# Kernel optimization log

Measured on AMD Instinct MI355X. Metric: run time of the kernel, lower is better.

## Reference

```python
import jax, jax.numpy as jnp
import numpy as np

OFFSET = 1  # self.offset

def setup_inputs() -> dict:
    key = jax.random.key(0)
    k1, k2, k3, k4, k5 = jax.random.split(key, 5)
    B, D, T, S, N = 16, 512, 1024, 12, 10
    x = jax.random.normal(k1, (B, D, T), dtype=jnp.float32)
    y = jax.random.normal(k2, (B, D, T), dtype=jnp.float32)
    W = jax.random.normal(k3, (D, D, S), dtype=jnp.float32) * 0.05  # ConvTranspose2d weight [in, out, 1, steps] squeezed
    b = jax.random.normal(k4, (D,), dtype=jnp.float32) * 0.05
    neg_idxs = jax.random.randint(k5, (B, N * T), 0, T)
    return {"x": x, "y": y, "W": W, "b": b, "neg_idxs": neg_idxs}


def reference(x, y, W, b, neg_idxs):
    B, F, T = y.shape
    N = neg_idxs.shape[1] // T
    # --- sample_negatives: gather by computed index over flattened y ---
    y_flat = jnp.transpose(y, (1, 0, 2)).reshape(F, B * T)          # [F, B*T]
    idx = (neg_idxs + jnp.arange(B, dtype=neg_idxs.dtype)[:, None] * T).reshape(-1)
    negs = y_flat[:, idx].reshape(F, B, N, T).transpose(2, 1, 0, 3)  # [N, B, F, T]
    targets = jnp.concatenate([y[None], negs], axis=0)               # [C=N+1, B, F, T]
    # --- project_to_steps: ConvTranspose2d with kernel (1, steps) == per-step linear ---
    xp = jnp.einsum('bit,ios->bots', x, W) + b[None, :, None, None]  # [B, F, T, S]
    C = N + 1
    S = xp.shape[-1]
    steps = min(S, T - OFFSET)
    preds, labels = [], []
    for i in range(steps):  # small fixed loop over prediction steps
        off = i + OFFSET
        # [C, B, T-off]: dot over feature dim, copies broadcast over x
        p = jnp.einsum('bft,cbft->cbt', xp[:, :, :T - off, i], targets[:, :, :, off:])
        preds.append(p.reshape(-1))
        lab = jnp.zeros((C, B * (T - off)), dtype=xp.dtype).at[0].set(1.0)
        labels.append(lab.reshape(-1))
    predictions = jnp.concatenate(preds)
    labels_out = jnp.concatenate(labels)
    return predictions, labels_out
```

## Files before the change

### kernel.cpp

```cpp
#include <hip/hip_runtime.h>

typedef __bf16 bf16x8 __attribute__((ext_vector_type(8)));
typedef float f32x4 __attribute__((ext_vector_type(4)));

#define B_ 16
#define T_ 1024
#define D_ 512
#define S_ 12
#define C_ 11
static constexpr int P_TOTAL = 2148960;

__device__ __host__ inline constexpr int pred_base(int i) {
  return C_ * B_ * (T_ * i - (i * (i + 1)) / 2);
}

__device__ inline unsigned short f2bf(float f) {
  unsigned int u = __float_as_uint(f);
  u += 0x7FFF + ((u >> 16) & 1);
  return (unsigned short)(u >> 16);
}

__device__ inline void gld16(const void* g, void* l) {
  __builtin_amdgcn_global_load_lds(
      (const __attribute__((address_space(1))) void*)g,
      (__attribute__((address_space(3))) void*)l, 16, 0, 0);
}

__global__ __launch_bounds__(256) void prep_w(const float* __restrict__ W,
                                              unsigned short* __restrict__ wt) {
  __shared__ unsigned short tile[32][33][12];
  const int i0 = blockIdx.x * 32, o0 = blockIdx.y * 32;
#pragma unroll
  for (int q = 0; q < 48; ++q) {
    int idx = threadIdx.x + q * 256;
    int ii = idx / 384, rem = idx % 384;
    tile[ii][rem / 12][rem % 12] =
        f2bf(W[(size_t)(i0 + ii) * 6144 + (size_t)o0 * 12 + rem]);
  }
  __syncthreads();
#pragma unroll
  for (int q = 0; q < 48; ++q) {
    int idx = threadIdx.x + q * 256;
    int ss = idx / 1024, rem = idx % 1024;
    int oo = rem / 32, ii = rem % 32;
    wt[(size_t)ss * (D_ * D_) + (size_t)(o0 + oo) * D_ + (i0 + ii)] = tile[ii][oo][ss];
  }
}

__global__ __launch_bounds__(256) void prep_t2(const float* __restrict__ xin,
                                               const float* __restrict__ yin,
                                               unsigned short* __restrict__ xo,
                                               unsigned short* __restrict__ yo) {
  __shared__ float tile[32][33];
  const int t0 = blockIdx.x * 32;
  const int d0 = blockIdx.y * 32;
  const int b = blockIdx.z & 15;
  const float* in = (blockIdx.z < 16) ? xin : yin;
  unsigned short* ob = (blockIdx.z < 16) ? xo : yo;
  const float* ib = in + (size_t)b * D_ * T_;
  const int r = threadIdx.x / 32, c = threadIdx.x % 32;
#pragma unroll
  for (int p = 0; p < 4; ++p) {
    int rr = r + p * 8;
    tile[rr][c] = ib[(size_t)(d0 + rr) * T_ + t0 + c];
  }
  __syncthreads();
  unsigned short* op = ob + (size_t)b * T_ * D_;
#pragma unroll
  for (int p = 0; p < 4; ++p) {
    int rr = r + p * 8;
    op[(size_t)(t0 + rr) * D_ + d0 + c] = f2bf(tile[c][rr]);
  }
}

__global__ void labels_k(float* __restrict__ lab) {
  int k = blockIdx.x * 256 + threadIdx.x;
  if (k >= P_TOTAL) return;
  int i = 0;
#pragma unroll
  for (int q = 1; q < 12; ++q)
    if (k >= pred_base(q)) i = q;
  int rel = k - pred_base(i);
  int len = T_ - 1 - i;
  lab[k] = (rel < B_ * len) ? 1.0f : 0.0f;
}

__global__ __launch_bounds__(512, 2) void gemm_xp(
    const unsigned short* __restrict__ xb,
    const unsigned short* __restrict__ wt,
    const float* __restrict__ bias,
    unsigned short* __restrict__ xp,
    int tiles, int mtiles) {
  __shared__ unsigned short lds[65536];
  const int tid = threadIdx.x;
  const int w = tid >> 6, l = tid & 63;
  const int gm = w >> 2, gn = w & 3;
  const int fr = l & 15, sgrp = l >> 4;

  const int so0 = tid * 16;
  const int row0 = so0 >> 6, sc0 = (so0 >> 4) & 3;
  const int go0 = row0 * 1024 + ((sc0 ^ ((row0 >> 1) & 3)) << 4);
  const int so1 = so0 + 8192;
  const int row1 = so1 >> 6, sc1 = (so1 >> 4) & 3;
  const int go1 = row1 * 1024 + ((sc1 ^ ((row1 >> 1) & 3)) << 4);

  auto stage = [&](const unsigned short* srcKt, int slotShorts) {
    gld16((const char*)srcKt + go0, (char*)&lds[slotShorts] + so0);
    gld16((const char*)srcKt + go1, (char*)&lds[slotShorts] + so1);
  };

  int aOff[2][4], bOff[4];
#pragma unroll
  for (int ms = 0; ms < 2; ++ms)
#pragma unroll
    for (int fm = 0; fm < 4; ++fm) {
      int row = gm * 128 + ms * 64 + fm * 16 + fr;
      aOff[ms][fm] = row * 32 + ((sgrp ^ ((row >> 1) & 3)) << 3);
    }
#pragma unroll
  for (int fn = 0; fn < 4; ++fn) {
    int row = gn * 64 + fn * 16 + fr;
    bOff[fn] = row * 32 + ((sgrp ^ ((row >> 1) & 3)) << 3);
  }

  auto decode = [&](int t, const unsigned short*& Ag, const unsigned short*& Bg,
                    int& n0v, int& miv, int& siv) {
    miv = t % mtiles;
    int rest = t / mtiles;
    int ni = rest & 1;
    siv = rest >> 1;
    Ag = xb + (size_t)(miv * 256) * D_;
    Bg = wt + ((size_t)siv * D_ + ni * 256) * D_;
    n0v = ni * 256;
  };

  int ti = blockIdx.x;
  if (ti >= tiles) return;
  const unsigned short *Ag, *Bg, *Agn = nullptr, *Bgn = nullptr;
  int n0, mi, si, n0n, min_, sin_;
  decode(ti, Ag, Bg, n0, mi, si);
  int tin = ti + gridDim.x;
  bool hasNext = tin < tiles;
  if (hasNext) decode(tin, Agn, Bgn, n0n, min_, sin_);

  stage(Ag, 0);
  stage(Bg, 8192);
  stage(Ag + 32, 16384);
  stage(Bg + 32, 16384 + 8192);
  asm volatile("s_waitcnt vmcnt(4)" ::: "memory");
  __builtin_amdgcn_s_barrier();

  bf16x8 afA[4], bfrA[4];
#pragma unroll
  for (int fn = 0; fn < 4; ++fn)
    bfrA[fn] = *(const bf16x8*)&lds[8192 + bOff[fn]];
#pragma unroll
  for (int fm = 0; fm < 4; ++fm)
    afA[fm] = *(const bf16x8*)&lds[aOff[0][fm]];

  while (true) {
    f32x4 acc[2][4][4];
#pragma unroll
    for (int ms = 0; ms < 2; ++ms)
#pragma unroll
      for (int fm = 0; fm < 4; ++fm)
#pragma unroll
        for (int fn = 0; fn < 4; ++fn)
#pragma unroll
          for (int e = 0; e < 4; ++e) acc[ms][fm][fn][e] = 0.f;

    float bv[4];
#pragma unroll
    for (int fn = 0; fn < 4; ++fn) bv[fn] = bias[n0 + gn * 64 + fn * 16 + fr];

#pragma unroll
    for (int kt = 0; kt < 16; ++kt) {
      const int sl = (kt & 3) * 16384;
      bf16x8 afB[4];
#pragma unroll
      for (int fm = 0; fm < 4; ++fm)
        afB[fm] = *(const bf16x8*)&lds[sl + aOff[1][fm]];

      const int k2 = kt + 2;
      const int sl2 = (k2 & 3) * 16384;
      bool st = false;
      if (k2 < 16) {
        stage(Ag + k2 * 32, sl2);
        stage(Bg + k2 * 32, sl2 + 8192);
        st = true;
      } else if (hasNext) {
        stage(Agn + (k2 - 16) * 32, sl2);
        stage(Bgn + (k2 - 16) * 32, sl2 + 8192);
        st = true;
      }

      __builtin_amdgcn_s_setprio(1);
#pragma unroll
      for (int fm = 0; fm < 4; ++fm)
#pragma unroll
        for (int fn = 0; fn < 4; ++fn)
          acc[0][fm][fn] = __builtin_amdgcn_mfma_f32_16x16x32_bf16(
              afA[fm], bfrA[fn], acc[0][fm][fn], 0, 0, 0);
      __builtin_amdgcn_s_setprio(0);

      if (st) {
        asm volatile("s_waitcnt vmcnt(4)" ::: "memory");
      } else if (kt == 14) {
        asm volatile("s_waitcnt vmcnt(0)" ::: "memory");
      }
      __builtin_amdgcn_s_barrier();

      bf16x8 afN[4], bfN[4];
      const bool pre = (kt < 15) || hasNext;
      if (pre) {
        const int nsl = ((kt + 1) & 3) * 16384;
#pragma unroll
        for (int fn = 0; fn < 4; ++fn)
          bfN[fn] = *(const bf16x8*)&lds[nsl + 8192 + bOff[fn]];
#pragma unroll
        for (int fm = 0; fm < 4; ++fm)
          afN[fm] = *(const bf16x8*)&lds[nsl + aOff[0][fm]];
      }

      __builtin_amdgcn_s_setprio(1);
#pragma unroll
      for (int fm = 0; fm < 4; ++fm)
#pragma unroll
        for (int fn = 0; fn < 4; ++fn)
          acc[1][fm][fn] = __builtin_amdgcn_mfma_f32_16x16x32_bf16(
              afB[fm], bfrA[fn], acc[1][fm][fn], 0, 0, 0);
      __builtin_amdgcn_s_setprio(0);

      if (pre) {
#pragma unroll
        for (int fm = 0; fm < 4; ++fm) afA[fm] = afN[fm];
#pragma unroll
        for (int fn = 0; fn < 4; ++fn) bfrA[fn] = bfN[fn];
      }
    }

#pragma unroll
    for (int ms = 0; ms < 2; ++ms) {
#pragma unroll
      for (int fm = 0; fm < 4; ++fm) {
#pragma unroll
        for (int r = 0; r < 4; ++r) {
          int m = mi * 256 + gm * 128 + ms * 64 + fm * 16 + sgrp * 4 + r;
          int bl = m >> 10, t = m & 1023;
          size_t orow = (((size_t)bl * S_ + si) * T_ + t) * D_;
#pragma unroll
          for (int fn = 0; fn < 4; ++fn) {
            int o = n0 + gn * 64 + fn * 16 + fr;
            xp[orow + o] = f2bf(acc[ms][fm][fn][r] + bv[fn]);
          }
        }
      }
    }

    if (!hasNext) break;
    ti = tin;
    Ag = Agn; Bg = Bgn; n0 = n0n; mi = min_; si = sin_;
    tin = ti + gridDim.x;
    hasNext = tin < tiles;
    if (hasNext) decode(tin, Agn, Bgn, n0n, min_, sin_);
  }
}

__global__ __launch_bounds__(256) void pred_k(
    const unsigned short* __restrict__ xp,
    const unsigned short* __restrict__ yT,
    const int* __restrict__ negs,
    float* __restrict__ preds, int b0) {
  const int w = threadIdx.x >> 6, l = threadIdx.x & 63;
  const int bl = blockIdx.y;
  const int b = b0 + bl;
  const int fr = l & 15;
  const int koff = (l >> 4) * 8;

  const unsigned short* arow[4];
  const unsigned short* brow[4];
  int tts[4];
#pragma unroll
  for (int q = 0; q < 4; ++q) {
    int tt = blockIdx.x * 4 + w + q * 256;
    tts[q] = tt;
    int t = tt - 1 - fr;
    bool av = (fr < S_) && (t >= 0);
    arow[q] = xp + (((size_t)bl * S_ + (av ? fr : 0)) * T_ + (av ? t : 0)) * D_;
    int j = tt;
    if (fr >= 1 && fr <= 10) j = negs[b * (10 * T_) + (fr - 1) * T_ + tt];
    brow[q] = yT + ((size_t)b * T_ + j) * D_;
  }

  f32x4 acc[4];
#pragma unroll
  for (int q = 0; q < 4; ++q)
#pragma unroll
    for (int e = 0; e < 4; ++e) acc[q][e] = 0.f;

#pragma unroll
  for (int kk = 0; kk < 16; ++kk) {
#pragma unroll
    for (int q = 0; q < 4; ++q) {
      bf16x8 a = *(const bf16x8*)(arow[q] + kk * 32 + koff);
      bf16x8 bb = *(const bf16x8*)(brow[q] + kk * 32 + koff);
      acc[q] = __builtin_amdgcn_mfma_f32_16x16x32_bf16(a, bb, acc[q], 0, 0, 0);
    }
  }

#pragma unroll
  for (int q = 0; q < 4; ++q) {
#pragma unroll
    for (int r = 0; r < 4; ++r) {
      int ii = (l >> 4) * 4 + r;
      int to = tts[q] - 1 - ii;
      if (ii < S_ && fr < C_ && tts[q] >= 1 && to >= 0) {
        int len = T_ - 1 - ii;
        preds[pred_base(ii) + ((size_t)fr * B_ + b) * len + to] = acc[q][r];
      }
    }
  }
}

extern "C" void kernel_launch(void* const* d_in, const int* in_sizes, int n_in,
                              void* d_out, int out_size, void* d_ws, size_t ws_size,
                              hipStream_t stream) {
  (void)in_sizes; (void)n_in; (void)out_size;
  const float* x = (const float*)d_in[0];
  const float* y = (const float*)d_in[1];
  const float* W = (const float*)d_in[2];
  const float* bias = (const float*)d_in[3];
  const int* negs = (const int*)d_in[4];
  float* out = (float*)d_out;
  char* ws = (char*)d_ws;

  unsigned short* wt = (unsigned short*)ws;
  unsigned short* xb = (unsigned short*)(ws + 6291456);
  unsigned short* yT = (unsigned short*)(ws + 6291456 + 16777216);
  unsigned short* xp = (unsigned short*)(ws + 6291456 + 2 * 16777216);
  const size_t fixed = 6291456 + (size_t)2 * 16777216;
  const size_t xp_per_b = (size_t)S_ * T_ * D_ * 2;
  int nb = 1;
  if (ws_size > fixed) {
    size_t cap = (ws_size - fixed) / xp_per_b;
    nb = cap < 1 ? 1 : (cap > 16 ? 16 : (int)cap);
  }

  hipLaunchKernelGGL(prep_w, dim3(16, 16), dim3(256), 0, stream, W, wt);
  hipLaunchKernelGGL(prep_t2, dim3(32, 16, 32), dim3(256), 0, stream, x, y, xb, yT);
  hipLaunchKernelGGL(labels_k, dim3((P_TOTAL + 255) / 256), dim3(256), 0, stream,
                     out + P_TOTAL);

  for (int b0 = 0; b0 < B_; b0 += nb) {
    int bc = (B_ - b0) < nb ? (B_ - b0) : nb;
    int tiles = bc * 4 * 2 * 12;
    int grid = tiles < 256 ? tiles : 256;
    hipLaunchKernelGGL(gemm_xp, dim3(grid), dim3(512), 0, stream,
                       xb + (size_t)b0 * T_ * D_, wt, bias, xp,
                       tiles, bc * 4);
    hipLaunchKernelGGL(pred_k, dim3(64, bc), dim3(256), 0, stream,
                       xp, yT, negs, out, b0);
  }
}
```

Baseline: 220.6 us.

## Retile projection GEMM to 256x128 tiles with XCD-aware scheduling and triple buffering

Shrinks the gemm_xp block from 512 to 256 threads and the output tile from 256x256 to 256x128. The LDS ring goes from four 32-wide K stages to three 64-wide stages (72 KB), so two blocks can fit per CU. Tile indices are reordered so each XCD handles a contiguous chunk of M-major tiles, aiming for better L2 reuse of the weights and activations. The cost is more tiles, with A loaded twice as often per output column, and different register and LDS pressure.

Result: slower. 259.2 us (+17.5%).

```diff
diff --git a/kernel.cpp b/kernel.cpp
--- a/kernel.cpp
+++ b/kernel.cpp
@@ -85,78 +85,96 @@
   lab[k] = (rel < B_ * len) ? 1.0f : 0.0f;
 }
 
-__global__ __launch_bounds__(512, 2) void gemm_xp(
+__global__ __launch_bounds__(256, 2) void gemm_xp(
     const unsigned short* __restrict__ xb,
     const unsigned short* __restrict__ wt,
     const float* __restrict__ bias,
     unsigned short* __restrict__ xp,
-    int tiles, int mtiles) {
-  __shared__ unsigned short lds[65536];
+    int tiles, int chunk, int bpx) {
+  __shared__ unsigned short lds[36864];
   const int tid = threadIdx.x;
   const int w = tid >> 6, l = tid & 63;
-  const int gm = w >> 2, gn = w & 3;
+  const int gm = w >> 1, gn = w & 1;
   const int fr = l & 15, sgrp = l >> 4;
 
-  const int so0 = tid * 16;
-  const int row0 = so0 >> 6, sc0 = (so0 >> 4) & 3;
-  const int go0 = row0 * 1024 + ((sc0 ^ ((row0 >> 1) & 3)) << 4);
-  const int so1 = so0 + 8192;
-  const int row1 = so1 >> 6, sc1 = (so1 >> 4) & 3;
-  const int go1 = row1 * 1024 + ((sc1 ^ ((row1 >> 1) & 3)) << 4);
-
-  auto stage = [&](const unsigned short* srcKt, int slotShorts) {
-    gld16((const char*)srcKt + go0, (char*)&lds[slotShorts] + so0);
-    gld16((const char*)srcKt + go1, (char*)&lds[slotShorts] + so1);
+  int soA[4], goA[4], soB[2], goB[2];
+#pragma unroll
+  for (int seg = 0; seg < 4; ++seg) {
+    soA[seg] = tid * 16 + seg * 4096;
+    int row = soA[seg] >> 6, sc = (soA[seg] >> 4) & 3;
+    goA[seg] = row * 1024 + ((sc ^ ((row >> 1) & 3)) << 4);
+  }
+#pragma unroll
+  for (int seg = 0; seg < 2; ++seg) {
+    soB[seg] = tid * 16 + seg * 4096;
+    int row = soB[seg] >> 6, sc = (soB[seg] >> 4) & 3;
+    goB[seg] = row * 1024 + ((sc ^ ((row >> 1) & 3)) << 4);
+  }
+
+  auto stage = [&](const unsigned short* Akt, const unsigned short* Bkt, int slotB) {
+#pragma unroll
+    for (int seg = 0; seg < 4; ++seg)
+      gld16((const char*)Akt + goA[seg], (char*)lds + slotB + soA[seg]);
+#pragma unroll
+    for (int seg = 0; seg < 2; ++seg)
+      gld16((const char*)Bkt + goB[seg], (char*)lds + slotB + 16384 + soB[seg]);
   };
 
-  int aOff[2][4], bOff[4];
-#pragma unroll
-  for (int ms = 0; ms < 2; ++ms)
-#pragma unroll
-    for (int fm = 0; fm < 4; ++fm) {
-      int row = gm * 128 + ms * 64 + fm * 16 + fr;
-      aOff[ms][fm] = row * 32 + ((sgrp ^ ((row >> 1) & 3)) << 3);
-    }
+  int aOff[8], bOff[4];
+#pragma unroll
+  for (int fm = 0; fm < 8; ++fm) {
+    int row = gm * 128 + fm * 16 + fr;
+    aOff[fm] = row * 64 + ((sgrp ^ ((row >> 1) & 3)) << 4);
+  }
 #pragma unroll
   for (int fn = 0; fn < 4; ++fn) {
     int row = gn * 64 + fn * 16 + fr;
-    bOff[fn] = row * 32 + ((sgrp ^ ((row >> 1) & 3)) << 3);
-  }
+    bOff[fn] = 16384 + row * 64 + ((sgrp ^ ((row >> 1) & 3)) << 4);
+  }
+
+  auto rdf = [&](int slotB, int off) -> bf16x8 {
+    return *(const bf16x8*)((const char*)lds + slotB + off);
+  };
 
   auto decode = [&](int t, const unsigned short*& Ag, const unsigned short*& Bg,
                     int& n0v, int& miv, int& siv) {
-    miv = t % mtiles;
-    int rest = t / mtiles;
-    int ni = rest & 1;
-    siv = rest >> 1;
+    miv = t / 48;
+    int r = t % 48;
+    int ni = r & 3;
+    siv = r >> 2;
     Ag = xb + (size_t)(miv * 256) * D_;
-    Bg = wt + ((size_t)siv * D_ + ni * 256) * D_;
-    n0v = ni * 256;
+    Bg = wt + ((size_t)siv * D_ + ni * 128) * D_;
+    n0v = ni * 128;
   };
 
-  int ti = blockIdx.x;
-  if (ti >= tiles) return;
+  const int xcd = blockIdx.x & 7;
+  const int idx = blockIdx.x >> 3;
+  const int limit = (xcd + 1) * chunk;
+  int ti = xcd * chunk + idx;
+  if (ti >= limit || ti >= tiles) return;
+
   const unsigned short *Ag, *Bg, *Agn = nullptr, *Bgn = nullptr;
   int n0, mi, si, n0n, min_, sin_;
   decode(ti, Ag, Bg, n0, mi, si);
-  int tin = ti + gridDim.x;
-  bool hasNext = tin < tiles;
+  int tin = ti + bpx;
+  bool hasNext = tin < limit;
   if (hasNext) decode(tin, Agn, Bgn, n0n, min_, sin_);
 
-  stage(Ag, 0);
-  stage(Bg, 8192);
-  stage(Ag + 32, 16384);
-  stage(Bg + 32, 16384 + 8192);
-  asm volatile("s_waitcnt vmcnt(4)" ::: "memory");
+  int rdB = 0, stB = 2 * 24576;
+  auto adv = [](int s) { return s == 2 * 24576 ? 0 : s + 24576; };
+
+  stage(Ag, Bg, 0);
+  stage(Ag + 32, Bg + 32, 24576);
+  asm volatile("s_waitcnt vmcnt(6)" ::: "memory");
   __builtin_amdgcn_s_barrier();
 
-  bf16x8 afA[4], bfrA[4];
-#pragma unroll
-  for (int fn = 0; fn < 4; ++fn)
-    bfrA[fn] = *(const bf16x8*)&lds[8192 + bOff[fn]];
-#pragma unroll
-  for (int fm = 0; fm < 4; ++fm)
-    afA[fm] = *(const bf16x8*)&lds[aOff[0][fm]];
+  bf16x8 afA[4], afB[4], bfrA[4];
+#pragma unroll
+  for (int fm = 0; fm < 4; ++fm) afA[fm] = rdf(0, aOff[fm]);
+#pragma unroll
+  for (int fm = 0; fm < 4; ++fm) afB[fm] = rdf(0, aOff[4 + fm]);
+#pragma unroll
+  for (int fn = 0; fn < 4; ++fn) bfrA[fn] = rdf(0, bOff[fn]);
 
   while (true) {
     f32x4 acc[2][4][4];
@@ -175,22 +193,12 @@
 
 #pragma unroll
     for (int kt = 0; kt < 16; ++kt) {
-      const int sl = (kt & 3) * 16384;
-      bf16x8 afB[4];
-#pragma unroll
-      for (int fm = 0; fm < 4; ++fm)
-        afB[fm] = *(const bf16x8*)&lds[sl + aOff[1][fm]];
-
-      const int k2 = kt + 2;
-      const int sl2 = (k2 & 3) * 16384;
       bool st = false;
-      if (k2 < 16) {
-        stage(Ag + k2 * 32, sl2);
-        stage(Bg + k2 * 32, sl2 + 8192);
+      if (kt < 14) {
+        stage(Ag + (kt + 2) * 32, Bg + (kt + 2) * 32, stB);
         st = true;
       } else if (hasNext) {
-        stage(Agn + (k2 - 16) * 32, sl2);
-        stage(Bgn + (k2 - 16) * 32, sl2 + 8192);
+        stage(Agn + (kt - 14) * 32, Bgn + (kt - 14) * 32, stB);
         st = true;
       }
 
@@ -204,22 +212,22 @@
       __builtin_amdgcn_s_setprio(0);
 
       if (st) {
-        asm volatile("s_waitcnt vmcnt(4)" ::: "memory");
+        asm volatile("s_waitcnt vmcnt(6)" ::: "memory");
       } else if (kt == 14) {
         asm volatile("s_waitcnt vmcnt(0)" ::: "memory");
       }
       __builtin_amdgcn_s_barrier();
 
-      bf16x8 afN[4], bfN[4];
+      const int rdN = adv(rdB);
+      bf16x8 afAn[4], afBn[4], bfn[4];
       const bool pre = (kt < 15) || hasNext;
       if (pre) {
-        const int nsl = ((kt + 1) & 3) * 16384;
-#pragma unroll
-        for (int fn = 0; fn < 4; ++fn)
-          bfN[fn] = *(const bf16x8*)&lds[nsl + 8192 + bOff[fn]];
-#pragma unroll
-        for (int fm = 0; fm < 4; ++fm)
-          afN[fm] = *(const bf16x8*)&lds[nsl + aOff[0][fm]];
+#pragma unroll
+        for (int fm = 0; fm < 4; ++fm) afAn[fm] = rdf(rdN, aOff[fm]);
+#pragma unroll
+        for (int fn = 0; fn < 4; ++fn) bfn[fn] = rdf(rdN, bOff[fn]);
+#pragma unroll
+        for (int fm = 0; fm < 4; ++fm) afBn[fm] = rdf(rdN, aOff[4 + fm]);
       }
 
       __builtin_amdgcn_s_setprio(1);
@@ -233,10 +241,14 @@
 
       if (pre) {
 #pragma unroll
-        for (int fm = 0; fm < 4; ++fm) afA[fm] = afN[fm];
-#pragma unroll
-        for (int fn = 0; fn < 4; ++fn) bfrA[fn] = bfN[fn];
-      }
+        for (int fm = 0; fm < 4; ++fm) afA[fm] = afAn[fm];
+#pragma unroll
+        for (int fm = 0; fm < 4; ++fm) afB[fm] = afBn[fm];
+#pragma unroll
+        for (int fn = 0; fn < 4; ++fn) bfrA[fn] = bfn[fn];
+      }
+      rdB = rdN;
+      stB = adv(stB);
     }
 
 #pragma unroll
@@ -260,8 +272,8 @@
     if (!hasNext) break;
     ti = tin;
     Ag = Agn; Bg = Bgn; n0 = n0n; mi = min_; si = sin_;
-    tin = ti + gridDim.x;
-    hasNext = tin < tiles;
+    tin = ti + bpx;
+    hasNext = tin < limit;
     if (hasNext) decode(tin, Agn, Bgn, n0n, min_, sin_);
   }
 }
@@ -353,11 +365,13 @@
 
   for (int b0 = 0; b0 < B_; b0 += nb) {
     int bc = (B_ - b0) < nb ? (B_ - b0) : nb;
-    int tiles = bc * 4 * 2 * 12;
-    int grid = tiles < 256 ? tiles : 256;
-    hipLaunchKernelGGL(gemm_xp, dim3(grid), dim3(512), 0, stream,
+    int tiles = bc * 4 * 4 * 12;
+    int grid = tiles < 512 ? tiles : 512;
+    int chunk = tiles / 8;
+    int bpx = grid / 8;
+    hipLaunchKernelGGL(gemm_xp, dim3(grid), dim3(256), 0, stream,
                        xb + (size_t)b0 * T_ * D_, wt, bias, xp,
-                       tiles, bc * 4);
+                       tiles, chunk, bpx);
     hipLaunchKernelGGL(pred_k, dim3(64, bc), dim3(256), 0, stream,
                        xp, yT, negs, out, b0);
   }
```

## Restructure xp GEMM into 8-step K loop with quadrant-staged double buffering

Applied to the files above, without the earlier changes.

The xp projection GEMM moves from a 16-step K loop with 32-wide K slices and a 4-slot LDS ring to 8 steps of 64-wide K slices, using two 64KB double buffers (128KB LDS, one block per CU). Each K step is split into four quadrants of MFMAs, and a half-panel global-to-LDS load is issued between quadrants, so loads overlap compute at finer granularity. The warp-to-tile mapping and XOR swizzle change to match the 128-byte rows. The trade-off is lower occupancy (one block per CU instead of two) and many more barriers per K step.

New measurement: 211.6 us. 4.1% less time.

```diff
diff --git a/kernel.cpp b/kernel.cpp
--- a/kernel.cpp
+++ b/kernel.cpp
@@ -85,43 +85,40 @@
   lab[k] = (rel < B_ * len) ? 1.0f : 0.0f;
 }
 
-__global__ __launch_bounds__(512, 2) void gemm_xp(
+__global__ __launch_bounds__(512, 1) void gemm_xp(
     const unsigned short* __restrict__ xb,
     const unsigned short* __restrict__ wt,
     const float* __restrict__ bias,
     unsigned short* __restrict__ xp,
     int tiles, int mtiles) {
-  __shared__ unsigned short lds[65536];
+  __shared__ char ldsb[131072];
   const int tid = threadIdx.x;
   const int w = tid >> 6, l = tid & 63;
   const int gm = w >> 2, gn = w & 3;
   const int fr = l & 15, sgrp = l >> 4;
 
-  const int so0 = tid * 16;
-  const int row0 = so0 >> 6, sc0 = (so0 >> 4) & 3;
-  const int go0 = row0 * 1024 + ((sc0 ^ ((row0 >> 1) & 3)) << 4);
-  const int so1 = so0 + 8192;
-  const int row1 = so1 >> 6, sc1 = (so1 >> 4) & 3;
-  const int go1 = row1 * 1024 + ((sc1 ^ ((row1 >> 1) & 3)) << 4);
-
-  auto stage = [&](const unsigned short* srcKt, int slotShorts) {
-    gld16((const char*)srcKt + go0, (char*)&lds[slotShorts] + so0);
-    gld16((const char*)srcKt + go1, (char*)&lds[slotShorts] + so1);
+  const int dox0 = tid * 16, dox1 = tid * 16 + 8192;
+  const int rl0 = dox0 >> 7, rl1 = dox1 >> 7;
+  const int col = dox0 & 127;
+  const int sco0 = rl0 * 1024 + (col ^ ((rl0 & 7) << 4));
+  const int sco1 = rl1 * 1024 + (col ^ ((rl1 & 7) << 4));
+
+  auto stageH = [&](const char* panel, int ks, int half, int ldsBase) {
+    const char* s = panel + half * 131072 + ks * 128;
+    char* d = ldsb + ldsBase + half * 16384;
+    gld16(s + sco0, d + dox0);
+    gld16(s + sco1, d + dox1);
   };
 
-  int aOff[2][4], bOff[4];
-#pragma unroll
-  for (int ms = 0; ms < 2; ++ms)
-#pragma unroll
-    for (int fm = 0; fm < 4; ++fm) {
-      int row = gm * 128 + ms * 64 + fm * 16 + fr;
-      aOff[ms][fm] = row * 32 + ((sgrp ^ ((row >> 1) & 3)) << 3);
-    }
-#pragma unroll
-  for (int fn = 0; fn < 4; ++fn) {
-    int row = gn * 64 + fn * 16 + fr;
-    bOff[fn] = row * 32 + ((sgrp ^ ((row >> 1) & 3)) << 3);
-  }
+  const int sw = (fr & 7) << 4;
+  const int colk0 = (sgrp * 16) ^ sw;
+  const int colk1 = (64 + sgrp * 16) ^ sw;
+  const int aRowB = (gm * 64 + fr) * 128;
+  const int bRowB = 32768 + (gn * 32 + fr) * 128;
+
+  auto ldf = [&](int off) -> bf16x8 {
+    return *(const bf16x8*)(ldsb + off);
+  };
 
   auto decode = [&](int t, const unsigned short*& Ag, const unsigned short*& Bg,
                     int& n0v, int& miv, int& siv) {
@@ -143,116 +140,141 @@
   bool hasNext = tin < tiles;
   if (hasNext) decode(tin, Agn, Bgn, n0n, min_, sin_);
 
-  stage(Ag, 0);
-  stage(Bg, 8192);
-  stage(Ag + 32, 16384);
-  stage(Bg + 32, 16384 + 8192);
+#define BAR()  asm volatile("" ::: "memory"); __builtin_amdgcn_s_barrier(); \
+               asm volatile("" ::: "memory")
+
+  stageH((const char*)Ag, 0, 0, 0);
+  stageH((const char*)Bg, 0, 0, 32768);
+  stageH((const char*)Ag, 0, 1, 0);
+  stageH((const char*)Bg, 0, 1, 32768);
   asm volatile("s_waitcnt vmcnt(4)" ::: "memory");
-  __builtin_amdgcn_s_barrier();
-
-  bf16x8 afA[4], bfrA[4];
-#pragma unroll
-  for (int fn = 0; fn < 4; ++fn)
-    bfrA[fn] = *(const bf16x8*)&lds[8192 + bOff[fn]];
-#pragma unroll
-  for (int fm = 0; fm < 4; ++fm)
-    afA[fm] = *(const bf16x8*)&lds[aOff[0][fm]];
+  BAR();
 
   while (true) {
-    f32x4 acc[2][4][4];
-#pragma unroll
-    for (int ms = 0; ms < 2; ++ms)
-#pragma unroll
-      for (int fm = 0; fm < 4; ++fm)
-#pragma unroll
-        for (int fn = 0; fn < 4; ++fn)
-#pragma unroll
-          for (int e = 0; e < 4; ++e) acc[ms][fm][fn][e] = 0.f;
-
-    float bv[4];
-#pragma unroll
-    for (int fn = 0; fn < 4; ++fn) bv[fn] = bias[n0 + gn * 64 + fn * 16 + fr];
-
-#pragma unroll
-    for (int kt = 0; kt < 16; ++kt) {
-      const int sl = (kt & 3) * 16384;
-      bf16x8 afB[4];
-#pragma unroll
-      for (int fm = 0; fm < 4; ++fm)
-        afB[fm] = *(const bf16x8*)&lds[sl + aOff[1][fm]];
-
-      const int k2 = kt + 2;
-      const int sl2 = (k2 & 3) * 16384;
-      bool st = false;
-      if (k2 < 16) {
-        stage(Ag + k2 * 32, sl2);
-        stage(Bg + k2 * 32, sl2 + 8192);
-        st = true;
-      } else if (hasNext) {
-        stage(Agn + (k2 - 16) * 32, sl2);
-        stage(Bgn + (k2 - 16) * 32, sl2 + 8192);
-        st = true;
-      }
-
+    f32x4 acc[8][4];
+#pragma unroll
+    for (int a = 0; a < 8; ++a)
+#pragma unroll
+      for (int bq = 0; bq < 4; ++bq)
+#pragma unroll
+        for (int e = 0; e < 4; ++e) acc[a][bq][e] = 0.f;
+
+    float bv[2][2];
+#pragma unroll
+    for (int nh = 0; nh < 2; ++nh)
+#pragma unroll
+      for (int fn = 0; fn < 2; ++fn)
+        bv[nh][fn] = bias[n0 + gn * 32 + nh * 128 + fn * 16 + fr];
+
+#pragma unroll
+    for (int ks = 0; ks < 8; ++ks) {
+      const int bufB = (ks & 1) * 65536;
+      const int nbufB = bufB ^ 65536;
+      const bool st = (ks < 7) || hasNext;
+      const char* pA = (ks < 7) ? (const char*)Ag : (const char*)Agn;
+      const char* pB = (ks < 7) ? (const char*)Bg : (const char*)Bgn;
+      const int kn = (ks < 7) ? ks + 1 : 0;
+      bf16x8 af[2][4], b0[2][2], b1[2][2];
+
+#pragma unroll
+      for (int fm = 0; fm < 4; ++fm) {
+        af[0][fm] = ldf(bufB + aRowB + fm * 2048 + colk0);
+        af[1][fm] = ldf(bufB + aRowB + fm * 2048 + colk1);
+      }
+#pragma unroll
+      for (int fn = 0; fn < 2; ++fn) {
+        b0[0][fn] = ldf(bufB + bRowB + fn * 2048 + colk0);
+        b0[1][fn] = ldf(bufB + bRowB + fn * 2048 + colk1);
+      }
+      if (st) {
+        stageH(pA, kn, 0, nbufB);
+        asm volatile("s_waitcnt vmcnt(2)" ::: "memory");
+      } else {
+        asm volatile("s_waitcnt vmcnt(0)" ::: "memory");
+      }
+      BAR();
       __builtin_amdgcn_s_setprio(1);
 #pragma unroll
-      for (int fm = 0; fm < 4; ++fm)
-#pragma unroll
-        for (int fn = 0; fn < 4; ++fn)
-          acc[0][fm][fn] = __builtin_amdgcn_mfma_f32_16x16x32_bf16(
-              afA[fm], bfrA[fn], acc[0][fm][fn], 0, 0, 0);
+      for (int kk = 0; kk < 2; ++kk)
+#pragma unroll
+        for (int fm = 0; fm < 4; ++fm)
+#pragma unroll
+          for (int fn = 0; fn < 2; ++fn)
+            acc[fm][fn] = __builtin_amdgcn_mfma_f32_16x16x32_bf16(
+                af[kk][fm], b0[kk][fn], acc[fm][fn], 0, 0, 0);
       __builtin_amdgcn_s_setprio(0);
-
-      if (st) {
-        asm volatile("s_waitcnt vmcnt(4)" ::: "memory");
-      } else if (kt == 14) {
-        asm volatile("s_waitcnt vmcnt(0)" ::: "memory");
-      }
-      __builtin_amdgcn_s_barrier();
-
-      bf16x8 afN[4], bfN[4];
-      const bool pre = (kt < 15) || hasNext;
-      if (pre) {
-        const int nsl = ((kt + 1) & 3) * 16384;
-#pragma unroll
-        for (int fn = 0; fn < 4; ++fn)
-          bfN[fn] = *(const bf16x8*)&lds[nsl + 8192 + bOff[fn]];
+      BAR();
+
+#pragma unroll
+      for (int fn = 0; fn < 2; ++fn) {
+        b1[0][fn] = ldf(bufB + bRowB + 16384 + fn * 2048 + colk0);
+        b1[1][fn] = ldf(bufB + bRowB + 16384 + fn * 2048 + colk1);
+      }
+      if (st) stageH(pB, kn, 0, nbufB + 32768);
+      BAR();
+      __builtin_amdgcn_s_setprio(1);
+#pragma unroll
+      for (int kk = 0; kk < 2; ++kk)
 #pragma unroll
         for (int fm = 0; fm < 4; ++fm)
-          afN[fm] = *(const bf16x8*)&lds[nsl + aOff[0][fm]];
-      }
-
+#pragma unroll
+          for (int fn = 0; fn < 2; ++fn)
+            acc[fm][2 + fn] = __builtin_amdgcn_mfma_f32_16x16x32_bf16(
+                af[kk][fm], b1[kk][fn], acc[fm][2 + fn], 0, 0, 0);
+      __builtin_amdgcn_s_setprio(0);
+      BAR();
+
+#pragma unroll
+      for (int fm = 0; fm < 4; ++fm) {
+        af[0][fm] = ldf(bufB + aRowB + 16384 + fm * 2048 + colk0);
+        af[1][fm] = ldf(bufB + aRowB + 16384 + fm * 2048 + colk1);
+      }
+      if (st) stageH(pA, kn, 1, nbufB);
+      BAR();
       __builtin_amdgcn_s_setprio(1);
 #pragma unroll
-      for (int fm = 0; fm < 4; ++fm)
-#pragma unroll
-        for (int fn = 0; fn < 4; ++fn)
-          acc[1][fm][fn] = __builtin_amdgcn_mfma_f32_16x16x32_bf16(
-              afB[fm], bfrA[fn], acc[1][fm][fn], 0, 0, 0);
+      for (int kk = 0; kk < 2; ++kk)
+#pragma unroll
+        for (int fm = 0; fm < 4; ++fm)
+#pragma unroll
+          for (int fn = 0; fn < 2; ++fn)
+            acc[4 + fm][2 + fn] = __builtin_amdgcn_mfma_f32_16x16x32_bf16(
+                af[kk][fm], b1[kk][fn], acc[4 + fm][2 + fn], 0, 0, 0);
       __builtin_amdgcn_s_setprio(0);
-
-      if (pre) {
-#pragma unroll
-        for (int fm = 0; fm < 4; ++fm) afA[fm] = afN[fm];
-#pragma unroll
-        for (int fn = 0; fn < 4; ++fn) bfrA[fn] = bfN[fn];
-      }
+      BAR();
+
+      if (st) stageH(pB, kn, 1, nbufB + 32768);
+      BAR();
+      __builtin_amdgcn_s_setprio(1);
+#pragma unroll
+      for (int kk = 0; kk < 2; ++kk)
+#pragma unroll
+        for (int fm = 0; fm < 4; ++fm)
+#pragma unroll
+          for (int fn = 0; fn < 2; ++fn)
+            acc[4 + fm][fn] = __builtin_amdgcn_mfma_f32_16x16x32_bf16(
+                af[kk][fm], b0[kk][fn], acc[4 + fm][fn], 0, 0, 0);
+      __builtin_amdgcn_s_setprio(0);
+      if (st) asm volatile("s_waitcnt vmcnt(4)" ::: "memory");
+      BAR();
     }
 
 #pragma unroll
-    for (int ms = 0; ms < 2; ++ms) {
+    for (int mh = 0; mh < 2; ++mh) {
 #pragma unroll
       for (int fm = 0; fm < 4; ++fm) {
 #pragma unroll
         for (int r = 0; r < 4; ++r) {
-          int m = mi * 256 + gm * 128 + ms * 64 + fm * 16 + sgrp * 4 + r;
+          int m = mi * 256 + gm * 64 + mh * 128 + fm * 16 + sgrp * 4 + r;
           int bl = m >> 10, t = m & 1023;
           size_t orow = (((size_t)bl * S_ + si) * T_ + t) * D_;
 #pragma unroll
-          for (int fn = 0; fn < 4; ++fn) {
-            int o = n0 + gn * 64 + fn * 16 + fr;
-            xp[orow + o] = f2bf(acc[ms][fm][fn][r] + bv[fn]);
-          }
+          for (int nh = 0; nh < 2; ++nh)
+#pragma unroll
+            for (int fn = 0; fn < 2; ++fn) {
+              int o = n0 + gn * 32 + nh * 128 + fn * 16 + fr;
+              xp[orow + o] = f2bf(acc[mh * 4 + fm][nh * 2 + fn][r] + bv[nh][fn]);
+            }
         }
       }
     }
@@ -264,6 +286,7 @@
     hasNext = tin < tiles;
     if (hasNext) decode(tin, Agn, Bgn, n0n, min_, sin_);
   }
+#undef BAR
 }
 
 __global__ __launch_bounds__(256) void pred_k(
```
